# Kernel tuning notes

Measured on AMD Instinct MI355X. Metric: run time of the kernel, lower is better.

## Reference

```python
import jax, jax.numpy as jnp
import numpy as np

IN_FEATURES = 256
N_HEADS = 4
N_HIDDEN = 128  # out_features, concat=False
SLOPE = 0.1
NEG_INF = -9e15


def setup_inputs() -> dict:
    key = jax.random.key(0)
    k1, k2, k3, k4 = jax.random.split(key, 4)
    N = 8192
    h = jax.random.normal(k1, (N, IN_FEATURES), dtype=jnp.float32)
    adj_mat = jax.random.randint(k2, (N, N), 0, 2, dtype=jnp.int32)
    # xavier_normal with gain=1.414
    std_W = 1.414 * (2.0 / (IN_FEATURES + N_HIDDEN * N_HEADS)) ** 0.5
    W = jax.random.normal(k3, (IN_FEATURES, N_HIDDEN * N_HEADS), dtype=jnp.float32) * std_W
    std_a = 1.414 * (2.0 / (2 * N_HIDDEN + 1)) ** 0.5
    a = jax.random.normal(k4, (N_HEADS, 2 * N_HIDDEN, 1), dtype=jnp.float32) * std_a
    return {"h": h, "adj_mat": adj_mat, "W": W, "a": a}


def reference(h, adj_mat, W, a):
    N = h.shape[0]
    # linear projection -> [H, N, d]
    ht = (h @ W).reshape(N, N_HEADS, N_HIDDEN).transpose(1, 0, 2)
    # dropout is identity (eval / p effectively 0), then LeakyReLU
    ht = jnp.where(ht >= 0, ht, SLOPE * ht)
    # additive attention scores: src[h,i] + tgt[h,j]
    src = jnp.einsum('hnd,hd->hn', ht, a[:, :N_HIDDEN, 0])  # [H, N]
    tgt = jnp.einsum('hnd,hd->hn', ht, a[:, N_HIDDEN:, 0])  # [H, N]
    e = src[:, :, None] + tgt[:, None, :]                   # [H, N, N]
    e = jnp.where(adj_mat[None, :, :] > 0, e, NEG_INF)
    attn = jax.nn.softmax(e, axis=-1)
    # weighted sum and mean over heads (concat=False)
    out = jnp.einsum('hnm,hmd->hnd', attn, ht).mean(axis=0)  # [N, d]
    return out
```

## Files before the change

### kernel.cpp

```cpp
#include <hip/hip_runtime.h>


typedef unsigned short u16;
typedef unsigned int u32;
using bf16x8 = __attribute__((ext_vector_type(8))) short;
using f32x4  = __attribute__((ext_vector_type(4))) float;
using i32x4  = __attribute__((ext_vector_type(4))) int;

__device__ __forceinline__ u16 f2bf(float f) {
  u32 u = __float_as_uint(f);
  return (u16)((u + 0x7FFFu + ((u >> 16) & 1u)) >> 16);
}
__device__ __forceinline__ float bf2f(u16 u) {
  return __uint_as_float(((u32)u) << 16);
}

__global__ void transpose_w(const float* __restrict__ W, float* __restrict__ Wt) {
  __shared__ float tile[32][33];
  int cb = blockIdx.x * 32, kb = blockIdx.y * 32;
  int tc = threadIdx.x & 31, tr = threadIdx.x >> 5;
  for (int p = 0; p < 32; p += 8)
    tile[tr + p][tc] = W[(size_t)(kb + tr + p) * 512 + cb + tc];
  __syncthreads();
  for (int p = 0; p < 32; p += 8)
    Wt[(size_t)(cb + tr + p) * 256 + kb + tc] = tile[tc][tr + p];
}

__global__ void ht_gemm(const float* __restrict__ h, const float* __restrict__ Wt,
                        u16* __restrict__ HT) {
  __shared__ __align__(16) u16 Abuf[128 * 40];
  __shared__ __align__(16) u16 Bbuf[128 * 40];
  int tid = threadIdx.x;
  int cb = blockIdx.x, rb = blockIdx.y;
  int r0 = rb * 128, c0 = cb * 128;
  int lane = tid & 63, wv = tid >> 6;
  int wr = wv >> 1, wc = wv & 1;
  int mrow = lane & 15, q = lane >> 4;
  int ch = tid & 7, m0 = tid >> 3;

  f32x4 acc[4][4];
#pragma unroll
  for (int i = 0; i < 4; i++)
#pragma unroll
    for (int j = 0; j < 4; j++) acc[i][j] = f32x4{0.f, 0.f, 0.f, 0.f};

  for (int kt = 0; kt < 256; kt += 32) {
    __syncthreads();
#pragma unroll
    for (int mp = 0; mp < 128; mp += 32) {
      int m = m0 + mp;
      float4 v = *(const float4*)(&h[(size_t)(r0 + m) * 256 + kt + ch * 4]);
      uint2 p;
      p.x = (u32)f2bf(v.x) | ((u32)f2bf(v.y) << 16);
      p.y = (u32)f2bf(v.z) | ((u32)f2bf(v.w) << 16);
      *(uint2*)(&Abuf[m * 40 + ch * 4]) = p;
      float4 u = *(const float4*)(&Wt[(size_t)(c0 + m) * 256 + kt + ch * 4]);
      uint2 r;
      r.x = (u32)f2bf(u.x) | ((u32)f2bf(u.y) << 16);
      r.y = (u32)f2bf(u.z) | ((u32)f2bf(u.w) << 16);
      *(uint2*)(&Bbuf[m * 40 + ch * 4]) = r;
    }
    __syncthreads();
    bf16x8 af[4], bfv[4];
#pragma unroll
    for (int i = 0; i < 4; i++)
      af[i] = *(const bf16x8*)(&Abuf[(wr * 64 + i * 16 + mrow) * 40 + q * 8]);
#pragma unroll
    for (int j = 0; j < 4; j++)
      bfv[j] = *(const bf16x8*)(&Bbuf[(wc * 64 + j * 16 + mrow) * 40 + q * 8]);
#pragma unroll
    for (int i = 0; i < 4; i++)
#pragma unroll
      for (int j = 0; j < 4; j++)
        acc[i][j] = __builtin_amdgcn_mfma_f32_16x16x32_bf16(af[i], bfv[j], acc[i][j], 0, 0, 0);
  }
#pragma unroll
  for (int i = 0; i < 4; i++)
#pragma unroll
    for (int j = 0; j < 4; j++)
#pragma unroll
      for (int r = 0; r < 4; r++) {
        int gi = r0 + wr * 64 + i * 16 + q * 4 + r;
        int gc = c0 + wc * 64 + j * 16 + mrow;
        float v = acc[i][j][r];
        v = v >= 0.f ? v : 0.1f * v;
        HT[(size_t)gi * 512 + gc] = f2bf(v);
      }
}

__global__ void build_yt(const u16* __restrict__ HT, const float* __restrict__ a,
                         u16* __restrict__ Yt) {
  __shared__ u16 sht[32][528];
  __shared__ float swv[32 * 4];
  __shared__ float sa[512];
  int t = threadIdx.x;
  int j0 = blockIdx.x * 32;
  for (int i = t; i < 512; i += 256) {
    int g = i >> 7, d = i & 127;
    sa[i] = a[g * 256 + 128 + d];
  }
#pragma unroll
  for (int p = 0; p < 8; ++p) {
    int el = t + 256 * p;
    int row = el >> 6, col8 = el & 63;
    *(uint4*)(&sht[row][col8 * 8]) = *(const uint4*)(&HT[(size_t)(j0 + row) * 512 + col8 * 8]);
  }
  __syncthreads();
  if (t < 128) {
    int jl = t >> 2, g = t & 3;
    float acc = 0.f;
#pragma unroll
    for (int d8 = 0; d8 < 16; ++d8) {
      bf16x8 v = *(const bf16x8*)(&sht[jl][g * 128 + d8 * 8]);
#pragma unroll
      for (int u = 0; u < 8; ++u)
        acc += bf2f((u16)v[u]) * sa[g * 128 + d8 * 8 + u];
    }
    swv[jl * 4 + g] = __expf(acc);
  }
  __syncthreads();
  int oj = (t & 3) * 8, oc = t >> 2;
  size_t T = j0 >> 5;
  for (int pass = 0; pass < 9; ++pass) {
    int c = pass * 64 + oc;
    if (c >= 528) break;
    u32 pk[4] = {0u, 0u, 0u, 0u};
    if (c < 512) {
      int g = c >> 7;
#pragma unroll
      for (int u = 0; u < 4; ++u) {
        int j = oj + 2 * u;
        float v0 = bf2f(sht[j][c]) * swv[j * 4 + g];
        float v1 = bf2f(sht[j + 1][c]) * swv[(j + 1) * 4 + g];
        pk[u] = (u32)f2bf(v0) | ((u32)f2bf(v1) << 16);
      }
    } else if (c < 516) {
      int g = c - 512;
#pragma unroll
      for (int u = 0; u < 4; ++u) {
        int j = oj + 2 * u;
        float v0 = swv[j * 4 + g];
        float v1 = swv[(j + 1) * 4 + g];
        pk[u] = (u32)f2bf(v0) | ((u32)f2bf(v1) << 16);
      }
    }
    size_t dst = ((size_t)(c >> 4) * 256 + T) * 512 + (size_t)(oj >> 3) * 128 + (c & 15) * 8;
    *(uint4*)(&Yt[dst]) = make_uint4(pk[0], pk[1], pk[2], pk[3]);
  }
}

__global__ __launch_bounds__(512) void adj_gemm(const int* __restrict__ adj,
                                                const u16* __restrict__ Yt,
                                                float* __restrict__ C,
                                                float* __restrict__ S) {
  __shared__ __align__(16) u16 Abuf[2][128 * 32];
  int tid = threadIdx.x;
  int rb = blockIdx.y, kh = blockIdx.x;
  int r0 = rb * 128, k0 = kh * 2048;
  int lane = tid & 63, wv = tid >> 6;
  int wr = wv >> 2, wc = wv & 3;
  int mrow = lane & 15, q = lane >> 4;
  int qs = q ^ ((mrow >> 1) & 3);
  int am = tid >> 2, aq = tid & 3;
  int asw = am * 32 + ((aq ^ ((am >> 1) & 3)) * 8);
  const int* abase = &adj[(size_t)(r0 + am) * 8192 + k0 + aq * 8];
  bool do_den = (wc == 0);
  const u16* ybase = Yt + ((size_t)(wc * 8) * 256 + (k0 >> 5)) * 512 + (size_t)lane * 8;
  const u16* dbase = Yt + ((size_t)32 * 256 + (k0 >> 5)) * 512 + (size_t)lane * 8;

  f32x4 acc[4][8];
#pragma unroll
  for (int i = 0; i < 4; i++)
#pragma unroll
    for (int j = 0; j < 8; j++) acc[i][j] = f32x4{0.f, 0.f, 0.f, 0.f};
  f32x4 accD[4];
#pragma unroll
  for (int i = 0; i < 4; i++) accD[i] = f32x4{0.f, 0.f, 0.f, 0.f};

#define LOADA(V0, V1, TT)                                              \
  {                                                                    \
    const int* ap = abase + (size_t)(TT) * 32;                         \
    V0 = __builtin_nontemporal_load((const i32x4*)(ap));               \
    V1 = __builtin_nontemporal_load((const i32x4*)(ap + 4));           \
  }
#define PACKA(DST, V0, V1)                                             \
  {                                                                    \
    uint4 pk;                                                          \
    pk.x = 16256u * ((u32)V0[0] | ((u32)V0[1] << 16));                 \
    pk.y = 16256u * ((u32)V0[2] | ((u32)V0[3] << 16));                 \
    pk.z = 16256u * ((u32)V1[0] | ((u32)V1[1] << 16));                 \
    pk.w = 16256u * ((u32)V1[2] | ((u32)V1[3] << 16));                 \
    *(uint4*)((DST) + asw) = pk;                                       \
  }

  {
    i32x4 a0, a1;
    LOADA(a0, a1, 0);
    PACKA(&Abuf[0][0], a0, a1);
  }
  asm volatile("s_waitcnt lgkmcnt(0)" ::: "memory");
  __builtin_amdgcn_s_barrier();

  for (int t = 0; t < 64; ++t) {
    bf16x8 bfv[8];
#pragma unroll
    for (int j = 0; j < 8; j++)
      bfv[j] = *(const bf16x8*)(ybase + ((size_t)j * 256 + t) * 512);
    bf16x8 bd;
    if (do_den) bd = *(const bf16x8*)(dbase + (size_t)t * 512);
    i32x4 v0, v1;
    if (t < 63) LOADA(v0, v1, t + 1);
    bf16x8 af[4];
    const u16* Ab = &Abuf[t & 1][0];
#pragma unroll
    for (int i = 0; i < 4; i++)
      af[i] = *(const bf16x8*)(&Ab[(wr * 64 + i * 16 + mrow) * 32 + qs * 8]);
    __builtin_amdgcn_s_setprio(1);
#pragma unroll
    for (int j = 0; j < 8; j++)
#pragma unroll
      for (int i = 0; i < 4; i++)
        acc[i][j] = __builtin_amdgcn_mfma_f32_16x16x32_bf16(af[i], bfv[j], acc[i][j], 0, 0, 0);
    if (do_den) {
#pragma unroll
      for (int i = 0; i < 4; i++)
        accD[i] = __builtin_amdgcn_mfma_f32_16x16x32_bf16(af[i], bd, accD[i], 0, 0, 0);
    }
    __builtin_amdgcn_s_setprio(0);
    if (t < 63) PACKA(&Abuf[(t + 1) & 1][0], v0, v1);
    asm volatile("s_waitcnt lgkmcnt(0)" ::: "memory");
    __builtin_amdgcn_s_barrier();
  }
#undef LOADA
#undef PACKA

  float* Ck = C + (size_t)kh * 8192 * 512;
#pragma unroll
  for (int i = 0; i < 4; i++)
#pragma unroll
    for (int j = 0; j < 8; j++)
#pragma unroll
      for (int r = 0; r < 4; r++) {
        int gi = r0 + wr * 64 + i * 16 + q * 4 + r;
        int gc = wc * 128 + j * 16 + mrow;
        Ck[(size_t)gi * 512 + gc] = acc[i][j][r];
      }
  if (do_den && mrow < 4) {
    float* Sk = S + (size_t)kh * 4 * 8192;
#pragma unroll
    for (int i = 0; i < 4; i++)
#pragma unroll
      for (int r = 0; r < 4; r++) {
        int gi = r0 + wr * 64 + i * 16 + q * 4 + r;
        Sk[(size_t)mrow * 8192 + gi] = accD[i][r];
      }
  }
}

__global__ void finalize_gat(const float* __restrict__ C, const float* __restrict__ S,
                             float* __restrict__ out) {
  int idx = blockIdx.x * 256 + threadIdx.x;
  int i = idx >> 7, d = idx & 127;
  float s = 0.f;
#pragma unroll
  for (int g = 0; g < 4; ++g) {
    float num = 0.f, den = 0.f;
#pragma unroll
    for (int kh = 0; kh < 4; ++kh) {
      num += C[(size_t)kh * 8192 * 512 + (size_t)i * 512 + g * 128 + d];
      den += S[(size_t)kh * 4 * 8192 + (size_t)g * 8192 + i];
    }
    s += num / den;
  }
  out[idx] = 0.25f * s;
}

extern "C" void kernel_launch(void* const* d_in, const int* in_sizes, int n_in,
                              void* d_out, int out_size, void* d_ws, size_t ws_size,
                              hipStream_t stream) {
  const float* h   = (const float*)d_in[0];
  const int*   adj = (const int*)d_in[1];
  const float* W   = (const float*)d_in[2];
  const float* a   = (const float*)d_in[3];
  float* out = (float*)d_out;
  char* ws = (char*)d_ws;
  float* Wt = (float*)(ws + 0);
  u16*   HT = (u16*)(ws + 524288);
  u16*   Yt = (u16*)(ws + 8912896);
  float* C  = (float*)(ws + 17563648);
  float* S  = (float*)(ws + 84672512);

  transpose_w<<<dim3(16, 8), 256, 0, stream>>>(W, Wt);
  ht_gemm<<<dim3(4, 64), 256, 0, stream>>>(h, Wt, HT);
  build_yt<<<dim3(256), 256, 0, stream>>>(HT, a, Yt);
  adj_gemm<<<dim3(4, 64), 512, 0, stream>>>(adj, Yt, C, S);
  finalize_gat<<<dim3(4096), 256, 0, stream>>>(C, S, out);
}
```

Before: 467.6 us.

## Pre-pack adjacency into bitmasks and build MFMA A-fragments from bits in registers

```diff
diff --git a/kernel.cpp b/kernel.cpp
--- a/kernel.cpp
+++ b/kernel.cpp
@@ -13,6 +13,21 @@
 }
 __device__ __forceinline__ float bf2f(u16 u) {
   return __uint_as_float(((u32)u) << 16);
+}
+
+__global__ void pack_adj(const int* __restrict__ adj, u32* __restrict__ adjb) {
+  int idx = blockIdx.x * 256 + threadIdx.x;
+  const int* p = adj + (size_t)idx * 32;
+  u32 m = 0;
+#pragma unroll
+  for (int c = 0; c < 8; ++c) {
+    i32x4 v = __builtin_nontemporal_load((const i32x4*)(p + 4 * c));
+    m |= (v[0] != 0 ? 1u : 0u) << (4 * c);
+    m |= (v[1] != 0 ? 1u : 0u) << (4 * c + 1);
+    m |= (v[2] != 0 ? 1u : 0u) << (4 * c + 2);
+    m |= (v[3] != 0 ? 1u : 0u) << (4 * c + 3);
+  }
+  adjb[idx] = m;
 }
 
 __global__ void transpose_w(const float* __restrict__ W, float* __restrict__ Wt) {
@@ -149,24 +164,22 @@
   }
 }
 
-__global__ __launch_bounds__(512) void adj_gemm(const int* __restrict__ adj,
+__global__ __launch_bounds__(512) void adj_gemm(const u32* __restrict__ adjb,
                                                 const u16* __restrict__ Yt,
                                                 float* __restrict__ C,
                                                 float* __restrict__ S) {
-  __shared__ __align__(16) u16 Abuf[2][128 * 32];
   int tid = threadIdx.x;
   int rb = blockIdx.y, kh = blockIdx.x;
-  int r0 = rb * 128, k0 = kh * 2048;
+  int r0 = rb * 128;
+  int w0 = kh * 64;
   int lane = tid & 63, wv = tid >> 6;
   int wr = wv >> 2, wc = wv & 3;
   int mrow = lane & 15, q = lane >> 4;
-  int qs = q ^ ((mrow >> 1) & 3);
-  int am = tid >> 2, aq = tid & 3;
-  int asw = am * 32 + ((aq ^ ((am >> 1) & 3)) * 8);
-  const int* abase = &adj[(size_t)(r0 + am) * 8192 + k0 + aq * 8];
+  u32 sh = q * 8;
   bool do_den = (wc == 0);
-  const u16* ybase = Yt + ((size_t)(wc * 8) * 256 + (k0 >> 5)) * 512 + (size_t)lane * 8;
-  const u16* dbase = Yt + ((size_t)32 * 256 + (k0 >> 5)) * 512 + (size_t)lane * 8;
+  const u32* mbase = adjb + (size_t)(r0 + wr * 64 + mrow) * 256 + w0;
+  const u16* ybase = Yt + ((size_t)(wc * 8) * 256 + (size_t)w0) * 512 + (size_t)lane * 8;
+  const u16* dbase = Yt + ((size_t)32 * 256 + (size_t)w0) * 512 + (size_t)lane * 8;
 
   f32x4 acc[4][8];
 #pragma unroll
@@ -176,30 +189,6 @@
   f32x4 accD[4];
 #pragma unroll
   for (int i = 0; i < 4; i++) accD[i] = f32x4{0.f, 0.f, 0.f, 0.f};
-
-#define LOADA(V0, V1, TT)                                              \
-  {                                                                    \
-    const int* ap = abase + (size_t)(TT) * 32;                         \
-    V0 = __builtin_nontemporal_load((const i32x4*)(ap));               \
-    V1 = __builtin_nontemporal_load((const i32x4*)(ap + 4));           \
-  }
-#define PACKA(DST, V0, V1)                                             \
-  {                                                                    \
-    uint4 pk;                                                          \
-    pk.x = 16256u * ((u32)V0[0] | ((u32)V0[1] << 16));                 \
-    pk.y = 16256u * ((u32)V0[2] | ((u32)V0[3] << 16));                 \
-    pk.z = 16256u * ((u32)V1[0] | ((u32)V1[1] << 16));                 \
-    pk.w = 16256u * ((u32)V1[2] | ((u32)V1[3] << 16));                 \
-    *(uint4*)((DST) + asw) = pk;                                       \
-  }
-
-  {
-    i32x4 a0, a1;
-    LOADA(a0, a1, 0);
-    PACKA(&Abuf[0][0], a0, a1);
-  }
-  asm volatile("s_waitcnt lgkmcnt(0)" ::: "memory");
-  __builtin_amdgcn_s_barrier();
 
   for (int t = 0; t < 64; ++t) {
     bf16x8 bfv[8];
@@ -208,13 +197,18 @@
       bfv[j] = *(const bf16x8*)(ybase + ((size_t)j * 256 + t) * 512);
     bf16x8 bd;
     if (do_den) bd = *(const bf16x8*)(dbase + (size_t)t * 512);
-    i32x4 v0, v1;
-    if (t < 63) LOADA(v0, v1, t + 1);
     bf16x8 af[4];
-    const u16* Ab = &Abuf[t & 1][0];
-#pragma unroll
-    for (int i = 0; i < 4; i++)
-      af[i] = *(const bf16x8*)(&Ab[(wr * 64 + i * 16 + mrow) * 32 + qs * 8]);
+#pragma unroll
+    for (int i = 0; i < 4; i++) {
+      u32 m = mbase[(size_t)i * 4096 + t];
+      u32 b = (m >> sh) & 0xFFu;
+      u32 w[4];
+#pragma unroll
+      for (int e = 0; e < 4; ++e)
+        w[e] = (((b >> (2 * e)) & 1u) ? 0x3F80u : 0u) |
+               (((b >> (2 * e + 1)) & 1u) ? 0x3F800000u : 0u);
+      af[i] = *(const bf16x8*)&w[0];
+    }
     __builtin_amdgcn_s_setprio(1);
 #pragma unroll
     for (int j = 0; j < 8; j++)
@@ -227,12 +221,7 @@
         accD[i] = __builtin_amdgcn_mfma_f32_16x16x32_bf16(af[i], bd, accD[i], 0, 0, 0);
     }
     __builtin_amdgcn_s_setprio(0);
-    if (t < 63) PACKA(&Abuf[(t + 1) & 1][0], v0, v1);
-    asm volatile("s_waitcnt lgkmcnt(0)" ::: "memory");
-    __builtin_amdgcn_s_barrier();
-  }
-#undef LOADA
-#undef PACKA
+  }
 
   float* Ck = C + (size_t)kh * 8192 * 512;
 #pragma unroll
@@ -289,10 +278,12 @@
   u16*   Yt = (u16*)(ws + 8912896);
   float* C  = (float*)(ws + 17563648);
   float* S  = (float*)(ws + 84672512);
-
+  u32*  adjb = (u32*)(ws + 84803584);
+
+  pack_adj<<<dim3(8192), 256, 0, stream>>>(adj, adjb);
   transpose_w<<<dim3(16, 8), 256, 0, stream>>>(W, Wt);
   ht_gemm<<<dim3(4, 64), 256, 0, stream>>>(h, Wt, HT);
   build_yt<<<dim3(256), 256, 0, stream>>>(HT, a, Yt);
-  adj_gemm<<<dim3(4, 64), 512, 0, stream>>>(adj, Yt, C, S);
+  adj_gemm<<<dim3(4, 64), 512, 0, stream>>>(adjb, Yt, C, S);
   finalize_gat<<<dim3(4096), 256, 0, stream>>>(C, S, out);
 }
```

New measurement: 552.4 us. 1.18x slower.
